# Optimization experiments

Hardware: AMD Instinct MI355X
Metric: run time of the kernel (lower is better)

Reference implementation:

```python
import jax, jax.numpy as jnp
import numpy as np

OWN_DIM = 7
INTR_DIM = 5
N_HEADS = 3
HEAD_DIM = 5
N_INTR = 256
ACT_DIM = 2
HID = 256
B = 16384


def setup_inputs() -> dict:
    key = jax.random.key(0)
    ks = jax.random.split(key, 16)
    def rn(k, shape, scale=0.1):
        return (jax.random.normal(k, shape, dtype=jnp.float32) * scale)
    obs = jax.random.normal(ks[0], (B, OWN_DIM + N_INTR * INTR_DIM), dtype=jnp.float32)
    in_dim = OWN_DIM + N_HEADS * HEAD_DIM  # 22
    return {
        "obs": obs,
        "Wq": rn(ks[1], (N_HEADS, HEAD_DIM, OWN_DIM)),
        "bq": rn(ks[2], (N_HEADS, HEAD_DIM)),
        "Wk": rn(ks[3], (N_HEADS, HEAD_DIM, INTR_DIM)),
        "bk": rn(ks[4], (N_HEADS, HEAD_DIM)),
        "Wv": rn(ks[5], (N_HEADS, HEAD_DIM, INTR_DIM)),
        "bv": rn(ks[6], (N_HEADS, HEAD_DIM)),
        "v_att": rn(ks[7], (N_HEADS, HEAD_DIM), 0.5),
        "temperature": jnp.ones((1,), dtype=jnp.float32) * 3.0,
        "W1": rn(ks[8], (in_dim, HID)),
        "b1": rn(ks[9], (HID,)),
        "W2": rn(ks[10], (HID, HID)),
        "b2": rn(ks[11], (HID,)),
        "Wf": rn(ks[12], (HID, ACT_DIM)),
        "bf": rn(ks[13], (ACT_DIM,)),
        "log_std": jnp.zeros((ACT_DIM,), dtype=jnp.float32),
    }


def reference(obs, Wq, bq, Wk, bk, Wv, bv, v_att, temperature,
              W1, b1, W2, b2, Wf, bf, log_std):
    own = obs[:, :OWN_DIM]                                   # [B,7]
    intr = obs[:, OWN_DIM:OWN_DIM + N_INTR * INTR_DIM].reshape(-1, N_INTR, INTR_DIM)  # [B,N,5]

    # per-head projections, all heads at once
    q = jnp.einsum('bo,hdo->bhd', own, Wq) + bq[None]        # [B,H,5]
    k = jnp.einsum('bni,hdi->bhnd', intr, Wk) + bk[None, :, None, :]  # [B,H,N,5]
    v = jnp.einsum('bni,hdi->bhnd', intr, Wv) + bv[None, :, None, :]  # [B,H,N,5]

    energy = jnp.tanh(q[:, :, None, :] + k)                  # [B,H,N,5]
    scores = jnp.einsum('bhnd,hd->bhn', energy, v_att)       # [B,H,N]
    scores = scores * jnp.abs(temperature)[0]

    is_padding = jnp.sum(jnp.abs(intr), axis=2) < 1e-6       # [B,N]
    scores = jnp.where(is_padding[:, None, :], -jnp.inf, scores)
    alpha = jax.nn.softmax(scores, axis=-1)                  # [B,H,N]
    alpha = jnp.nan_to_num(alpha, nan=0.0)

    context = jnp.einsum('bhn,bhnd->bhd', alpha, v).reshape(-1, N_HEADS * HEAD_DIM)  # [B,15]

    x = jnp.concatenate([own, context], axis=1)              # [B,22]
    x = jax.nn.leaky_relu(x @ W1 + b1, negative_slope=0.2)
    x = jax.nn.leaky_relu(x @ W2 + b2, negative_slope=0.2)
    out = x @ Wf + bf                                        # [B,2]
    log_std_exp = jnp.broadcast_to(log_std[None, :], (out.shape[0], ACT_DIM))
    return jnp.concatenate([out, log_std_exp], axis=1)       # [B,4]
```

## Files before the change

### kernel.cpp

```cpp
#include <hip/hip_runtime.h>
#include <hip/hip_bf16.h>
#include <math.h>

#define OWN_DIM 7
#define INTR_DIM 5
#define N_HEADS 3
#define HEAD_DIM 5
#define N_INTR 256
#define HID 256
#define BATCH 16384
#define ROW 1287

typedef __attribute__((ext_vector_type(8))) short bf16x8;
typedef __attribute__((ext_vector_type(4))) float f32x4;

__device__ __forceinline__ float leaky(float x) {
    return x > 0.0f ? x : 0.2f * x;
}

__device__ __forceinline__ unsigned short f2bf(float f) {
    union { float f; unsigned u; } v; v.f = f;
    unsigned r = (v.u + 0x7FFFu + ((v.u >> 16) & 1u)) >> 16;
    return (unsigned short)r;
}

__device__ __forceinline__ unsigned pkbf(float a, float b) {
    __hip_bfloat162 h2 = __float22bfloat162_rn(make_float2(a, b));
    unsigned u;
    __builtin_memcpy(&u, &h2, 4);
    return u;
}

__device__ __forceinline__ float rdlane(float v, int l) {
    int iv = __builtin_bit_cast(int, v);
    return __builtin_bit_cast(float, __builtin_amdgcn_readlane(iv, l));
}

__global__ __launch_bounds__(256, 4) void attn_kernel(
    const float* __restrict__ obs,
    const float* __restrict__ Wq, const float* __restrict__ bq,
    const float* __restrict__ Wk, const float* __restrict__ bk,
    const float* __restrict__ Wv, const float* __restrict__ bv,
    const float* __restrict__ v_att, const float* __restrict__ temperature,
    const float* __restrict__ W1, const float* __restrict__ W2,
    unsigned short* __restrict__ xb,
    unsigned short* __restrict__ W1t, unsigned short* __restrict__ W2t)
{
    __shared__ __align__(16) float srow[4 * ROW + 4];
    int tid = threadIdx.x;

    {
        const float4* src = (const float4*)(obs + (size_t)blockIdx.x * 4 * ROW);
        float4* dst = (float4*)srow;
        #pragma unroll
        for (int i = 0; i < 5; i++) dst[tid + 256 * i] = src[tid + 256 * i];
        if (tid < 7) dst[1280 + tid] = src[1280 + tid];
    }

    int waveu = __builtin_amdgcn_readfirstlane(tid >> 6);
    int lane = tid & 63;
    int b = blockIdx.x * 4 + waveu;
    const float* rowg = obs + (size_t)b * ROW;

    float absT = fabsf(temperature[0]);
    float own_s[7];
    #pragma unroll
    for (int o = 0; o < 7; o++) own_s[o] = rowg[o];

    int hd = lane < 15 ? lane : 14;
    float qv = bq[hd] + bk[hd];
    #pragma unroll
    for (int o = 0; o < 7; o++) qv = fmaf(own_s[o], Wq[hd * 7 + o], qv);
    qv *= 2.0f;
    float m2vav = -2.0f * absT * v_att[hd];

    float qb2[15], m2va[15];
    #pragma unroll
    for (int i = 0; i < 15; i++) {
        qb2[i] = rdlane(qv, i);
        m2va[i] = rdlane(m2vav, i);
    }
    float Sva[3];
    #pragma unroll
    for (int h = 0; h < 3; h++) {
        float s = 0.0f;
        #pragma unroll
        for (int d = 0; d < 5; d++) s += m2va[h * 5 + d];
        Sva[h] = -0.5f * s;
    }
    __syncthreads();

    const float* row = srow + waveu * ROW;

    float it[4][5];
    float asum[4];
    #pragma unroll
    for (int j = 0; j < 4; j++) {
        const float* ip = row + OWN_DIM + INTR_DIM * (lane + 64 * j);
        float a = 0.0f;
        #pragma unroll
        for (int i = 0; i < 5; i++) {
            float v = ip[i];
            it[j][i] = v + v;
            a += fabsf(v);
        }
        asum[j] = a;
    }

    float sc[3][4];
    #pragma unroll
    for (int j = 0; j < 4; j++) {
        bool pad = asum[j] < 1e-6f;
        #pragma unroll
        for (int h = 0; h < 3; h++) {
            float s = Sva[h];
            #pragma unroll
            for (int d = 0; d < 5; d++) {
                float y = qb2[h * 5 + d];
                #pragma unroll
                for (int i = 0; i < 5; i++)
                    y = fmaf(it[j][i], Wk[(h * 5 + d) * 5 + i], y);
                float t = __expf(y) + 1.0f;
                s = fmaf(m2va[h * 5 + d], __builtin_amdgcn_rcpf(t), s);
            }
            sc[h][j] = pad ? -INFINITY : s;
        }
    }

    float alpha[3][4];
    float sa[3];
    #pragma unroll
    for (int h = 0; h < 3; h++) {
        float m = fmaxf(fmaxf(sc[h][0], sc[h][1]), fmaxf(sc[h][2], sc[h][3]));
        #pragma unroll
        for (int off = 32; off >= 1; off >>= 1) m = fmaxf(m, __shfl_xor(m, off));
        if (m < -3.0e38f) m = 0.0f;
        float lsum = 0.0f;
        #pragma unroll
        for (int j = 0; j < 4; j++) { alpha[h][j] = __expf(sc[h][j] - m); lsum += alpha[h][j]; }
        #pragma unroll
        for (int off = 32; off >= 1; off >>= 1) lsum += __shfl_xor(lsum, off);
        float rden = lsum > 0.0f ? 0.5f * __builtin_amdgcn_rcpf(lsum) : 0.0f;
        sa[h] = lsum > 0.0f ? 1.0f : 0.0f;
        #pragma unroll
        for (int j = 0; j < 4; j++) alpha[h][j] *= rden;
    }

    float cp[15];
    #pragma unroll
    for (int i = 0; i < 15; i++) cp[i] = 0.0f;
    #pragma unroll
    for (int h = 0; h < 3; h++)
        #pragma unroll
        for (int j = 0; j < 4; j++) {
            float a = alpha[h][j];
            #pragma unroll
            for (int i = 0; i < 5; i++)
                cp[h * 5 + i] = fmaf(a, it[j][i], cp[h * 5 + i]);
        }
    float* red = srow + waveu * ROW;
    #pragma unroll
    for (int i = 0; i < 15; i++) red[lane * 17 + i] = cp[i];
    {
        int q4 = lane >> 4, ci = lane & 15;
        float ps = 0.0f;
        #pragma unroll
        for (int r = 0; r < 16; r++) ps += red[(q4 * 16 + r) * 17 + ci];
        ps += __shfl_xor(ps, 16);
        ps += __shfl_xor(ps, 32);
        if (lane < 15) red[1090 + lane] = ps;
    }
    float ctx[15];
    #pragma unroll
    for (int i = 0; i < 15; i++) ctx[i] = red[1090 + i];

    float x[22];
    #pragma unroll
    for (int o = 0; o < 7; o++) x[o] = own_s[o];
    #pragma unroll
    for (int k = 0; k < 15; k++) {
        int h = k / 5;
        float acc = bv[k] * sa[h];
        #pragma unroll
        for (int i = 0; i < 5; i++)
            acc = fmaf(Wv[k * 5 + i], ctx[h * 5 + i], acc);
        x[7 + k] = acc;
    }

    unsigned up[12];
    #pragma unroll
    for (int i = 0; i < 11; i++) up[i] = pkbf(x[2 * i], x[2 * i + 1]);
    up[11] = 0u;
    uint4 u0 = { up[0], up[1], up[2],  up[3] };
    uint4 u1 = { up[4], up[5], up[6],  up[7] };
    uint4 u2 = { up[8], up[9], up[10], up[11] };
    uint4 u3 = { 0u, 0u, 0u, 0u };
    uint4 lo = (lane & 1) ? u1 : u0;
    uint4 hi = (lane & 1) ? u3 : u2;
    uint4 sel = (lane & 2) ? hi : lo;
    if (lane < 4) {
        *((uint4*)(xb + (size_t)b * 32 + lane * 8)) = sel;
    }

    if (blockIdx.x < 64) {
        int idx = blockIdx.x * 256 + tid;
        int col = idx & 255;
        int kq = idx >> 8;
        ushort4 o;
        o.x = f2bf(W2[(kq * 4 + 0) * 256 + col]);
        o.y = f2bf(W2[(kq * 4 + 1) * 256 + col]);
        o.z = f2bf(W2[(kq * 4 + 2) * 256 + col]);
        o.w = f2bf(W2[(kq * 4 + 3) * 256 + col]);
        *((ushort4*)(W2t + col * 256 + kq * 4)) = o;
        if (kq < 8) {
            ushort4 p;
            int k = kq * 4;
            p.x = (k + 0) < 22 ? f2bf(W1[(k + 0) * 256 + col]) : 0;
            p.y = (k + 1) < 22 ? f2bf(W1[(k + 1) * 256 + col]) : 0;
            p.z = (k + 2) < 22 ? f2bf(W1[(k + 2) * 256 + col]) : 0;
            p.w = (k + 3) < 22 ? f2bf(W1[(k + 3) * 256 + col]) : 0;
            *((ushort4*)(W1t + col * 32 + k)) = p;
        }
    }
}

__global__ __launch_bounds__(256, 2) void mlp_fused_kernel(
    const unsigned short* __restrict__ xb,
    const unsigned short* __restrict__ W1t, const unsigned short* __restrict__ W2t,
    const float* __restrict__ b1, const float* __restrict__ b2,
    const float* __restrict__ Wf, const float* __restrict__ bfv,
    const float* __restrict__ log_std, float* __restrict__ out)
{
    __shared__ unsigned short h1t[16 * 264];
    __shared__ float finbuf[2][4][16][2];

    int tid = threadIdx.x;
    int w = tid >> 6;
    int lane = tid & 63;
    int lm = lane & 15;
    int q = lane >> 4;
    int mbase = blockIdx.x * 32;

    float b1v[4], b2v[4], wf0[4], wf1[4];
    bf16x8 fw1[4];
    bf16x8 fw2[4][8];
    #pragma unroll
    for (int s = 0; s < 4; s++) {
        int col = w * 64 + s * 16 + lm;
        b1v[s] = b1[col];
        b2v[s] = b2[col];
        wf0[s] = Wf[col * 2];
        wf1[s] = Wf[col * 2 + 1];
        fw1[s] = *((const bf16x8*)(W1t + col * 32 + q * 8));
        #pragma unroll
        for (int t = 0; t < 8; t++)
            fw2[s][t] = *((const bf16x8*)(W2t + col * 256 + t * 32 + q * 8));
    }

    #pragma unroll
    for (int mt = 0; mt < 2; mt++) {
        int m0 = mbase + mt * 16;
        bf16x8 ax = *((const bf16x8*)(xb + (size_t)(m0 + lm) * 32 + q * 8));

        #pragma unroll
        for (int s = 0; s < 4; s++) {
            f32x4 c = {0.0f, 0.0f, 0.0f, 0.0f};
            c = __builtin_amdgcn_mfma_f32_16x16x32_bf16(ax, fw1[s], c, 0, 0, 0);
            int col = w * 64 + s * 16 + lm;
            #pragma unroll
            for (int i = 0; i < 4; i++)
                h1t[(q * 4 + i) * 264 + col] = f2bf(leaky(c[i] + b1v[s]));
        }
        __syncthreads();

        bf16x8 a2[8];
        #pragma unroll
        for (int t = 0; t < 8; t++)
            a2[t] = *((const bf16x8*)(h1t + lm * 264 + t * 32 + q * 8));

        float p0[4] = {0, 0, 0, 0};
        float p1[4] = {0, 0, 0, 0};
        #pragma unroll
        for (int s = 0; s < 4; s++) {
            f32x4 acc = {0.0f, 0.0f, 0.0f, 0.0f};
            #pragma unroll
            for (int t = 0; t < 8; t++)
                acc = __builtin_amdgcn_mfma_f32_16x16x32_bf16(a2[t], fw2[s][t], acc, 0, 0, 0);
            #pragma unroll
            for (int i = 0; i < 4; i++) {
                float h2 = leaky(acc[i] + b2v[s]);
                p0[i] = fmaf(h2, wf0[s], p0[i]);
                p1[i] = fmaf(h2, wf1[s], p1[i]);
            }
        }

        #pragma unroll
        for (int off = 1; off < 16; off <<= 1) {
            #pragma unroll
            for (int i = 0; i < 4; i++) {
                p0[i] += __shfl_xor(p0[i], off);
                p1[i] += __shfl_xor(p1[i], off);
            }
        }
        if (lm == 0) {
            #pragma unroll
            for (int i = 0; i < 4; i++) {
                finbuf[mt][w][q * 4 + i][0] = p0[i];
                finbuf[mt][w][q * 4 + i][1] = p1[i];
            }
        }
        __syncthreads();
        if (tid < 32) {
            int r = tid >> 1;
            int a = tid & 1;
            float s4 = finbuf[mt][0][r][a] + finbuf[mt][1][r][a]
                     + finbuf[mt][2][r][a] + finbuf[mt][3][r][a];
            out[(size_t)(m0 + r) * 4 + a] = s4 + bfv[a];
            out[(size_t)(m0 + r) * 4 + 2 + a] = log_std[a];
        }
    }
}

extern "C" void kernel_launch(void* const* d_in, const int* in_sizes, int n_in,
                              void* d_out, int out_size, void* d_ws, size_t ws_size,
                              hipStream_t stream) {
    const float* obs  = (const float*)d_in[0];
    const float* Wq   = (const float*)d_in[1];
    const float* bq   = (const float*)d_in[2];
    const float* Wk   = (const float*)d_in[3];
    const float* bk   = (const float*)d_in[4];
    const float* Wv   = (const float*)d_in[5];
    const float* bv   = (const float*)d_in[6];
    const float* v_att = (const float*)d_in[7];
    const float* temperature = (const float*)d_in[8];
    const float* W1   = (const float*)d_in[9];
    const float* b1   = (const float*)d_in[10];
    const float* W2   = (const float*)d_in[11];
    const float* b2   = (const float*)d_in[12];
    const float* Wf   = (const float*)d_in[13];
    const float* bf   = (const float*)d_in[14];
    const float* log_std = (const float*)d_in[15];
    float* out = (float*)d_out;

    unsigned short* xb  = (unsigned short*)d_ws;
    unsigned short* W1t = xb + (size_t)BATCH * 32;
    unsigned short* W2t = W1t + 256 * 32;

    attn_kernel<<<BATCH / 4, 256, 0, stream>>>(
        obs, Wq, bq, Wk, bk, Wv, bv, v_att, temperature, W1, W2,
        xb, W1t, W2t);
    mlp_fused_kernel<<<BATCH / 32, 256, 0, stream>>>(
        xb, W1t, W2t, b1, b2, Wf, bf, log_std, out);
}
```

Measured before the change: 179.6 us.

## Split weight prep into separate kernel and simplify attention reductions

Moves the bf16 transpose of W1/W2 out of the attention kernel into a dedicated prep kernel launched first. In the attention kernel, the query projection is now computed redundantly per lane from shared memory instead of via readlane broadcasts. The LDS-based context reduction is replaced with 15 full butterfly shuffle reductions. This removes LDS traffic and the branch for the first 64 blocks, at the cost of an extra kernel launch, more per-thread FMAs, and 90 shuffles per wave.

```diff
diff --git a/kernel.cpp b/kernel.cpp
--- a/kernel.cpp
+++ b/kernel.cpp
@@ -31,9 +31,28 @@
     return u;
 }
 
-__device__ __forceinline__ float rdlane(float v, int l) {
-    int iv = __builtin_bit_cast(int, v);
-    return __builtin_bit_cast(float, __builtin_amdgcn_readlane(iv, l));
+__global__ __launch_bounds__(256) void prep_kernel(
+    const float* __restrict__ W1, const float* __restrict__ W2,
+    unsigned short* __restrict__ W1t, unsigned short* __restrict__ W2t)
+{
+    int idx = blockIdx.x * 256 + threadIdx.x;
+    int col = idx & 255;
+    int kq = idx >> 8;
+    ushort4 o;
+    o.x = f2bf(W2[(kq * 4 + 0) * 256 + col]);
+    o.y = f2bf(W2[(kq * 4 + 1) * 256 + col]);
+    o.z = f2bf(W2[(kq * 4 + 2) * 256 + col]);
+    o.w = f2bf(W2[(kq * 4 + 3) * 256 + col]);
+    *((ushort4*)(W2t + col * 256 + kq * 4)) = o;
+    if (kq < 8) {
+        ushort4 p;
+        int k = kq * 4;
+        p.x = (k + 0) < 22 ? f2bf(W1[(k + 0) * 256 + col]) : 0;
+        p.y = (k + 1) < 22 ? f2bf(W1[(k + 1) * 256 + col]) : 0;
+        p.z = (k + 2) < 22 ? f2bf(W1[(k + 2) * 256 + col]) : 0;
+        p.w = (k + 3) < 22 ? f2bf(W1[(k + 3) * 256 + col]) : 0;
+        *((ushort4*)(W1t + col * 32 + k)) = p;
+    }
 }
 
 __global__ __launch_bounds__(256, 4) void attn_kernel(
@@ -42,9 +61,7 @@
     const float* __restrict__ Wk, const float* __restrict__ bk,
     const float* __restrict__ Wv, const float* __restrict__ bv,
     const float* __restrict__ v_att, const float* __restrict__ temperature,
-    const float* __restrict__ W1, const float* __restrict__ W2,
-    unsigned short* __restrict__ xb,
-    unsigned short* __restrict__ W1t, unsigned short* __restrict__ W2t)
+    unsigned short* __restrict__ xb)
 {
     __shared__ __align__(16) float srow[4 * ROW + 4];
     int tid = threadIdx.x;
@@ -56,29 +73,27 @@
         for (int i = 0; i < 5; i++) dst[tid + 256 * i] = src[tid + 256 * i];
         if (tid < 7) dst[1280 + tid] = src[1280 + tid];
     }
-
-    int waveu = __builtin_amdgcn_readfirstlane(tid >> 6);
+    __syncthreads();
+
+    int wave = tid >> 6;
     int lane = tid & 63;
-    int b = blockIdx.x * 4 + waveu;
-    const float* rowg = obs + (size_t)b * ROW;
+    int b = blockIdx.x * 4 + wave;
+    const float* row = srow + wave * ROW;
 
     float absT = fabsf(temperature[0]);
-    float own_s[7];
-    #pragma unroll
-    for (int o = 0; o < 7; o++) own_s[o] = rowg[o];
-
-    int hd = lane < 15 ? lane : 14;
-    float qv = bq[hd] + bk[hd];
-    #pragma unroll
-    for (int o = 0; o < 7; o++) qv = fmaf(own_s[o], Wq[hd * 7 + o], qv);
-    qv *= 2.0f;
-    float m2vav = -2.0f * absT * v_att[hd];
+
+    float own[7];
+    #pragma unroll
+    for (int o = 0; o < 7; o++) own[o] = row[o];
 
     float qb2[15], m2va[15];
     #pragma unroll
-    for (int i = 0; i < 15; i++) {
-        qb2[i] = rdlane(qv, i);
-        m2va[i] = rdlane(m2vav, i);
+    for (int hd = 0; hd < 15; hd++) {
+        float acc = bq[hd] + bk[hd];
+        #pragma unroll
+        for (int o = 0; o < 7; o++) acc = fmaf(own[o], Wq[hd * 7 + o], acc);
+        qb2[hd] = acc + acc;
+        m2va[hd] = -2.0f * absT * v_att[hd];
     }
     float Sva[3];
     #pragma unroll
@@ -88,9 +103,6 @@
         for (int d = 0; d < 5; d++) s += m2va[h * 5 + d];
         Sva[h] = -0.5f * s;
     }
-    __syncthreads();
-
-    const float* row = srow + waveu * ROW;
 
     float it[4][5];
     float asum[4];
@@ -146,9 +158,9 @@
         for (int j = 0; j < 4; j++) alpha[h][j] *= rden;
     }
 
-    float cp[15];
-    #pragma unroll
-    for (int i = 0; i < 15; i++) cp[i] = 0.0f;
+    float ctx[15];
+    #pragma unroll
+    for (int i = 0; i < 15; i++) ctx[i] = 0.0f;
     #pragma unroll
     for (int h = 0; h < 3; h++)
         #pragma unroll
@@ -156,27 +168,19 @@
             float a = alpha[h][j];
             #pragma unroll
             for (int i = 0; i < 5; i++)
-                cp[h * 5 + i] = fmaf(a, it[j][i], cp[h * 5 + i]);
-        }
-    float* red = srow + waveu * ROW;
-    #pragma unroll
-    for (int i = 0; i < 15; i++) red[lane * 17 + i] = cp[i];
-    {
-        int q4 = lane >> 4, ci = lane & 15;
-        float ps = 0.0f;
-        #pragma unroll
-        for (int r = 0; r < 16; r++) ps += red[(q4 * 16 + r) * 17 + ci];
-        ps += __shfl_xor(ps, 16);
-        ps += __shfl_xor(ps, 32);
-        if (lane < 15) red[1090 + lane] = ps;
-    }
-    float ctx[15];
-    #pragma unroll
-    for (int i = 0; i < 15; i++) ctx[i] = red[1090 + i];
+                ctx[h * 5 + i] = fmaf(a, it[j][i], ctx[h * 5 + i]);
+        }
+    #pragma unroll
+    for (int hi = 0; hi < 15; hi++) {
+        float v = ctx[hi];
+        #pragma unroll
+        for (int off = 32; off >= 1; off >>= 1) v += __shfl_xor(v, off);
+        ctx[hi] = v;
+    }
 
     float x[22];
     #pragma unroll
-    for (int o = 0; o < 7; o++) x[o] = own_s[o];
+    for (int o = 0; o < 7; o++) x[o] = own[o];
     #pragma unroll
     for (int k = 0; k < 15; k++) {
         int h = k / 5;
@@ -200,27 +204,6 @@
     uint4 sel = (lane & 2) ? hi : lo;
     if (lane < 4) {
         *((uint4*)(xb + (size_t)b * 32 + lane * 8)) = sel;
-    }
-
-    if (blockIdx.x < 64) {
-        int idx = blockIdx.x * 256 + tid;
-        int col = idx & 255;
-        int kq = idx >> 8;
-        ushort4 o;
-        o.x = f2bf(W2[(kq * 4 + 0) * 256 + col]);
-        o.y = f2bf(W2[(kq * 4 + 1) * 256 + col]);
-        o.z = f2bf(W2[(kq * 4 + 2) * 256 + col]);
-        o.w = f2bf(W2[(kq * 4 + 3) * 256 + col]);
-        *((ushort4*)(W2t + col * 256 + kq * 4)) = o;
-        if (kq < 8) {
-            ushort4 p;
-            int k = kq * 4;
-            p.x = (k + 0) < 22 ? f2bf(W1[(k + 0) * 256 + col]) : 0;
-            p.y = (k + 1) < 22 ? f2bf(W1[(k + 1) * 256 + col]) : 0;
-            p.z = (k + 2) < 22 ? f2bf(W1[(k + 2) * 256 + col]) : 0;
-            p.w = (k + 3) < 22 ? f2bf(W1[(k + 3) * 256 + col]) : 0;
-            *((ushort4*)(W1t + col * 32 + k)) = p;
-        }
     }
 }
 
@@ -346,9 +329,9 @@
     unsigned short* W1t = xb + (size_t)BATCH * 32;
     unsigned short* W2t = W1t + 256 * 32;
 
+    prep_kernel<<<64, 256, 0, stream>>>(W1, W2, W1t, W2t);
     attn_kernel<<<BATCH / 4, 256, 0, stream>>>(
-        obs, Wq, bq, Wk, bk, Wv, bv, v_att, temperature, W1, W2,
-        xb, W1t, W2t);
+        obs, Wq, bq, Wk, bk, Wv, bv, v_att, temperature, xb);
     mlp_fused_kernel<<<BATCH / 32, 256, 0, stream>>>(
         xb, W1t, W2t, b1, b2, Wf, bf, log_std, out);
 }
```

Result: slower. 184.7 us (+2.8%).
